# Kernel tuning notes

Measured on AMD Instinct MI355X. Metric: run time of the kernel, lower is better.

The kernel has to match this reference:

```python
import jax, jax.numpy as jnp
import numpy as np

# PyTorch LSTM cell with zero initial (h, c): W_hh @ h0 == 0, and c = sigmoid(i)*tanh(g)
# since the forget-gate term f*c0 vanishes. Gate order in torch: i, f, g, o.
# b here is the combined b_ih + b_hh (identical math).

def lstm_step0(x, Wih, b):
    pre = x @ Wih.T + b                      # (N, 4H)
    i, f, g, o = jnp.split(pre, 4, axis=-1)
    c = jax.nn.sigmoid(i) * jnp.tanh(g)
    return jax.nn.sigmoid(o) * jnp.tanh(c)   # (N, H)


def setup_inputs() -> dict:
    key = jax.random.key(0)
    ks = jax.random.split(key, 13)
    num_ts, num_periods, F = 128, 256, 128
    GH, NH, NF = 512, 256, 10
    s = lambda k, shape, fan: (jax.random.normal(k, shape, jnp.float32) / np.sqrt(fan))
    return {
        "X": jax.random.normal(ks[0], (num_ts, num_periods, F), jnp.float32),
        "g_Wih0": s(ks[1], (4 * GH, F), F),
        "g_b0": s(ks[2], (4 * GH,), GH),
        "g_Wih1": s(ks[3], (4 * GH, GH), GH),
        "g_b1": s(ks[4], (4 * GH,), GH),
        "aff_W": s(ks[5], (NF, GH), GH),
        "aff_b": s(ks[6], (NF,), GH),
        "n_Wih0": s(ks[7], (4 * NH, F), F),
        "n_b0": s(ks[8], (4 * NH,), NH),
        "n_Wih1": s(ks[9], (4 * NH, NH), NH),
        "n_b1": s(ks[10], (4 * NH,), NH),
        "noise_W": s(ks[11], (1, NH), NH),
        "noise_b": s(ks[12], (1,), NH),
    }


def reference(X, g_Wih0, g_b0, g_Wih1, g_b1, aff_W, aff_b,
              n_Wih0, n_b0, n_Wih1, n_b1, noise_W, noise_b):
    num_ts, num_periods, num_feats = X.shape
    x = X.reshape(-1, num_feats)             # (num_ts*num_periods, F)

    # Global factor branch: 2-layer LSTM single step from zero state
    hg = lstm_step0(lstm_step0(x, g_Wih0, g_b0), g_Wih1, g_b1)
    hg = jax.nn.relu(hg)
    mus = (hg @ aff_W.T + aff_b).sum(axis=-1).reshape(num_ts, num_periods)

    # Noise branch: 2-layer LSTM single step from zero state
    hn = lstm_step0(lstm_step0(x, n_Wih0, n_b0), n_Wih1, n_b1)
    hn = jax.nn.relu(hn)
    sigmas = jax.nn.softplus(hn @ noise_W.T + noise_b)  # log(1+exp(.)), stable
    sigmas = sigmas.reshape(num_ts, num_periods) + 1e-6
    return mus, sigmas
```

## Files before the change

### kernel.cpp

```cpp
#include <hip/hip_runtime.h>
#include <hip/hip_bf16.h>
#include <hip/hip_fp16.h>

typedef _Float16 h8_t __attribute__((ext_vector_type(8)));
typedef _Float16 h4_t __attribute__((ext_vector_type(4)));
typedef float f4_t __attribute__((ext_vector_type(4)));

#define M_ROWS 32768

__device__ __forceinline__ void gload_lds16(const void* g, void* l) {
  __builtin_amdgcn_global_load_lds((const __attribute__((address_space(1))) void*)g,
                                   (__attribute__((address_space(3))) void*)l, 16, 0, 0);
}

__device__ __forceinline__ float sigmoid_f(float x) { return 1.f / (1.f + __expf(-x)); }
__device__ __forceinline__ float tanh_f(float x) { return 1.f - 2.f / (__expf(2.f * x) + 1.f); }

struct GArgs {
  const _Float16* A;
  const _Float16* W;
  const float* bias;
  _Float16* Hout;
  const float* rvec;
  float* partial;
};

__global__ void prep_all(const float* __restrict__ X, const float* __restrict__ gW0,
                         const float* __restrict__ gW1, const float* __restrict__ nW0,
                         const float* __restrict__ nW1, const float* __restrict__ aff_W,
                         const float* __restrict__ aff_b,
                         _Float16* __restrict__ Xh, _Float16* __restrict__ Wg0,
                         _Float16* __restrict__ Wg1, _Float16* __restrict__ Wn0,
                         _Float16* __restrict__ Wn1,
                         float* __restrict__ pg, float* __restrict__ pn,
                         float* __restrict__ wsum) {
  int b = blockIdx.x;
  const float* s; _Float16* d; int base;
  if (b < 4096)      { s = X;   d = Xh;  base = b; }
  else if (b < 4352) { s = gW0; d = Wg0; base = b - 4096; }
  else if (b < 5376) { s = gW1; d = Wg1; base = b - 4352; }
  else if (b < 5504) { s = nW0; d = Wn0; base = b - 5376; }
  else if (b < 5760) { s = nW1; d = Wn1; base = b - 5504; }
  else if (b < 5888) {
    int i = (b - 5760) * 256 + threadIdx.x;
    pg[i] = 0.f; pn[i] = 0.f;
    return;
  } else {
    int j = (b - 5888) * 256 + threadIdx.x;
    float sum = 0.f;
#pragma unroll
    for (int r = 0; r < 10; ++r) sum += aff_W[r * 512 + j];
    wsum[j] = sum;
    if (j == 0) {
      float bs = 0.f;
#pragma unroll
      for (int r = 0; r < 10; ++r) bs += aff_b[r];
      wsum[512] = bs;
    }
    return;
  }
  int i4 = (base * 256 + threadIdx.x) * 4;
  float4 v = *(const float4*)(s + i4);
  h4_t o;
  o[0] = (_Float16)v.x; o[1] = (_Float16)v.y; o[2] = (_Float16)v.z; o[3] = (_Float16)v.w;
  *(h4_t*)(d + i4) = o;
}

template <int K_DIM, int H_DIM, bool FUSE>
__device__ __forceinline__ void gemm_body(const GArgs& ga, int h0, int m0,
                                          _Float16* As, _Float16* Bs) {
  const int tid = threadIdx.x;
  const int wid = tid >> 6;
  const int lane = tid & 63;
  const int wave_m = wid >> 1;
  const int wave_h = wid & 1;
  const int q = lane >> 4;
  const int tcol = lane & 15;

  constexpr int NT = K_DIM / 64;
  constexpr int A_BYTES = 128 * 64 * 2;
  constexpr int B_BYTES = 3 * 64 * 64 * 2;
  constexpr int A_ELEMS = 128 * 64;
  constexpr int B_ELEMS = 3 * 64 * 64;

  const _Float16* aptr[4]; int aoff[4];
#pragma unroll
  for (int c = 0; c < 4; ++c) {
    int o = ((wid * 4 + c) << 10) + (lane << 4);
    int row = o >> 7, pch = (o >> 4) & 7;
    int lch = pch ^ (row & 7);
    aptr[c] = ga.A + (size_t)(m0 + row) * K_DIM + lch * 8;
    aoff[c] = o;
  }
  const _Float16* bptr[6]; int boff[6];
#pragma unroll
  for (int c = 0; c < 6; ++c) {
    int o = ((wid * 6 + c) << 10) + (lane << 4);
    int pan = o >> 13;
    int row = (o >> 7) & 63, pch = (o >> 4) & 7;
    int lch = pch ^ (row & 7);
    int gbase = (pan == 0 ? 0 : (pan == 1 ? 2 * H_DIM : 3 * H_DIM)) + h0 + row;
    bptr[c] = ga.W + (size_t)gbase * K_DIM + lch * 8;
    boff[c] = o;
  }
  int a_rd[2][4];
#pragma unroll
  for (int ks = 0; ks < 2; ++ks)
#pragma unroll
    for (int mi = 0; mi < 4; ++mi) {
      int r = wave_m * 64 + mi * 16 + tcol;
      int c = ks * 4 + q;
      a_rd[ks][mi] = r * 64 + (c ^ (r & 7)) * 8;
    }
  int b_rd[2][2];
#pragma unroll
  for (int ks = 0; ks < 2; ++ks)
#pragma unroll
    for (int ni = 0; ni < 2; ++ni) {
      int j = wave_h * 32 + ni * 16 + tcol;
      int c = ks * 4 + q;
      b_rd[ks][ni] = j * 64 + (c ^ (j & 7)) * 8;
    }

  f4_t acc[3][4][2];
#pragma unroll
  for (int p = 0; p < 3; ++p)
#pragma unroll
    for (int mi = 0; mi < 4; ++mi)
#pragma unroll
      for (int ni = 0; ni < 2; ++ni) acc[p][mi][ni] = (f4_t){0.f, 0.f, 0.f, 0.f};

#pragma unroll
  for (int c = 0; c < 4; ++c) gload_lds16(aptr[c], (char*)As + aoff[c]);
#pragma unroll
  for (int c = 0; c < 6; ++c) gload_lds16(bptr[c], (char*)Bs + boff[c]);
#pragma unroll
  for (int c = 0; c < 4; ++c) aptr[c] += 64;
#pragma unroll
  for (int c = 0; c < 6; ++c) bptr[c] += 64;

#pragma unroll
  for (int kk = 0; kk < NT; ++kk) {
    const int cur = kk & 1;
    const int nxt = cur ^ 1;
    if (kk < NT - 1) {
#pragma unroll
      for (int c = 0; c < 4; ++c) gload_lds16(aptr[c], (char*)As + nxt * A_BYTES + aoff[c]);
#pragma unroll
      for (int c = 0; c < 6; ++c) gload_lds16(bptr[c], (char*)Bs + nxt * B_BYTES + boff[c]);
#pragma unroll
      for (int c = 0; c < 4; ++c) aptr[c] += 64;
#pragma unroll
      for (int c = 0; c < 6; ++c) bptr[c] += 64;
      asm volatile("s_waitcnt vmcnt(10)" ::: "memory");
    } else {
      asm volatile("s_waitcnt vmcnt(0)" ::: "memory");
    }
    __builtin_amdgcn_s_barrier();
    asm volatile("" ::: "memory");

#pragma unroll
    for (int ks = 0; ks < 2; ++ks) {
      h8_t af[4];
#pragma unroll
      for (int mi = 0; mi < 4; ++mi) af[mi] = *(const h8_t*)&As[cur * A_ELEMS + a_rd[ks][mi]];
#pragma unroll
      for (int p = 0; p < 3; ++p) {
#pragma unroll
        for (int ni = 0; ni < 2; ++ni) {
          h8_t bf = *(const h8_t*)&Bs[cur * B_ELEMS + p * 4096 + b_rd[ks][ni]];
#pragma unroll
          for (int mi = 0; mi < 4; ++mi)
            acc[p][mi][ni] = __builtin_amdgcn_mfma_f32_16x16x32_f16(af[mi], bf, acc[p][mi][ni], 0, 0, 0);
        }
      }
    }
    asm volatile("" ::: "memory");
    if (kk < NT - 1) __builtin_amdgcn_s_barrier();
  }

  const int mrow0 = m0 + wave_m * 64;
  const int jcol0 = h0 + wave_h * 32;

  if constexpr (!FUSE) {
#pragma unroll
    for (int ni = 0; ni < 2; ++ni) {
      int j = jcol0 + ni * 16 + tcol;
      float bi = ga.bias[j];
      float bg = ga.bias[2 * H_DIM + j];
      float bo = ga.bias[3 * H_DIM + j];
#pragma unroll
      for (int mi = 0; mi < 4; ++mi)
#pragma unroll
        for (int r = 0; r < 4; ++r) {
          float pi = acc[0][mi][ni][r] + bi;
          float pgt = acc[1][mi][ni][r] + bg;
          float po = acc[2][mi][ni][r] + bo;
          float cc = sigmoid_f(pi) * tanh_f(pgt);
          float hh = sigmoid_f(po) * tanh_f(cc);
          int m = mrow0 + mi * 16 + q * 4 + r;
          ga.Hout[(size_t)m * H_DIM + j] = (_Float16)hh;
        }
    }
  } else {
    float rsum[4][4];
#pragma unroll
    for (int mi = 0; mi < 4; ++mi)
#pragma unroll
      for (int r = 0; r < 4; ++r) rsum[mi][r] = 0.f;
#pragma unroll
    for (int ni = 0; ni < 2; ++ni) {
      int j = jcol0 + ni * 16 + tcol;
      float bi = ga.bias[j];
      float bg = ga.bias[2 * H_DIM + j];
      float bo = ga.bias[3 * H_DIM + j];
      float rv = ga.rvec[j];
#pragma unroll
      for (int mi = 0; mi < 4; ++mi)
#pragma unroll
        for (int r = 0; r < 4; ++r) {
          float pi = acc[0][mi][ni][r] + bi;
          float pgt = acc[1][mi][ni][r] + bg;
          float po = acc[2][mi][ni][r] + bo;
          float cc = sigmoid_f(pi) * tanh_f(pgt);
          float hh = sigmoid_f(po) * tanh_f(cc);
          hh = fmaxf(hh, 0.f);
          rsum[mi][r] += hh * rv;
        }
    }
#pragma unroll
    for (int mi = 0; mi < 4; ++mi)
#pragma unroll
      for (int r = 0; r < 4; ++r) {
        float v = rsum[mi][r];
        v += __shfl_xor(v, 1);
        v += __shfl_xor(v, 2);
        v += __shfl_xor(v, 4);
        v += __shfl_xor(v, 8);
        if (tcol == 0) atomicAdd(&ga.partial[mrow0 + mi * 16 + q * 4 + r], v);
      }
  }
}

__device__ __forceinline__ void swizzle_xy(int& x, int& y) {
  int lin = blockIdx.y * gridDim.x + blockIdx.x;
  int c = lin & 7;
  int r = lin >> 3;
  y = r % 12;
  x = c * 32 + r / 12;
}

__global__ __launch_bounds__(256, 2) void layer1_fused(GArgs g, GArgs n) {
  __shared__ __align__(16) _Float16 As[2 * 128 * 64];
  __shared__ __align__(16) _Float16 Bs[2 * 3 * 64 * 64];
  int x, y; swizzle_xy(x, y);
  if (y < 8) gemm_body<128, 512, false>(g, y * 64, x * 128, As, Bs);
  else       gemm_body<128, 256, false>(n, (y - 8) * 64, x * 128, As, Bs);
}

__global__ __launch_bounds__(256, 2) void layer2_fused(GArgs g, GArgs n) {
  __shared__ __align__(16) _Float16 As[2 * 128 * 64];
  __shared__ __align__(16) _Float16 Bs[2 * 3 * 64 * 64];
  int x, y; swizzle_xy(x, y);
  if (y < 8) gemm_body<512, 512, true>(g, y * 64, x * 128, As, Bs);
  else       gemm_body<256, 256, true>(n, (y - 8) * 64, x * 128, As, Bs);
}

__global__ void finalize(const float* __restrict__ pg, const float* __restrict__ pn,
                         const float* __restrict__ wsum, const float* __restrict__ noise_b,
                         float* __restrict__ out) {
  int i = blockIdx.x * blockDim.x + threadIdx.x;
  out[i] = pg[i] + wsum[512];
  float x = pn[i] + noise_b[0];
  float sp = fmaxf(x, 0.f) + log1pf(expf(-fabsf(x)));
  out[M_ROWS + i] = sp + 1e-6f;
}

extern "C" void kernel_launch(void* const* d_in, const int* in_sizes, int n_in,
                              void* d_out, int out_size, void* d_ws, size_t ws_size,
                              hipStream_t stream) {
  const float* X       = (const float*)d_in[0];
  const float* g_Wih0  = (const float*)d_in[1];
  const float* g_b0    = (const float*)d_in[2];
  const float* g_Wih1  = (const float*)d_in[3];
  const float* g_b1    = (const float*)d_in[4];
  const float* aff_W   = (const float*)d_in[5];
  const float* aff_b   = (const float*)d_in[6];
  const float* n_Wih0  = (const float*)d_in[7];
  const float* n_b0    = (const float*)d_in[8];
  const float* n_Wih1  = (const float*)d_in[9];
  const float* n_b1    = (const float*)d_in[10];
  const float* noise_W = (const float*)d_in[11];
  const float* noise_b = (const float*)d_in[12];
  float* out = (float*)d_out;

  char* w = (char*)d_ws;
  _Float16* Xh  = (_Float16*)w; w += (size_t)M_ROWS * 128 * 2;
  _Float16* Wg0 = (_Float16*)w; w += 2048 * 128 * 2;
  _Float16* Wg1 = (_Float16*)w; w += 2048 * 512 * 2;
  _Float16* Wn0 = (_Float16*)w; w += 1024 * 128 * 2;
  _Float16* Wn1 = (_Float16*)w; w += 1024 * 256 * 2;
  _Float16* h1g = (_Float16*)w; w += (size_t)M_ROWS * 512 * 2;
  _Float16* h1n = (_Float16*)w; w += (size_t)M_ROWS * 256 * 2;
  float* pg   = (float*)w; w += (size_t)M_ROWS * 4;
  float* pn   = (float*)w; w += (size_t)M_ROWS * 4;
  float* wsum = (float*)w; w += 4096;

  prep_all<<<5890, 256, 0, stream>>>(X, g_Wih0, g_Wih1, n_Wih0, n_Wih1, aff_W, aff_b,
                                     Xh, Wg0, Wg1, Wn0, Wn1, pg, pn, wsum);

  GArgs l1g = {Xh, Wg0, g_b0, h1g, nullptr, nullptr};
  GArgs l1n = {Xh, Wn0, n_b0, h1n, nullptr, nullptr};
  layer1_fused<<<dim3(M_ROWS / 128, 12), 256, 0, stream>>>(l1g, l1n);

  GArgs l2g = {h1g, Wg1, g_b1, nullptr, wsum, pg};
  GArgs l2n = {h1n, Wn1, n_b1, nullptr, noise_W, pn};
  layer2_fused<<<dim3(M_ROWS / 128, 12), 256, 0, stream>>>(l2g, l2n);

  finalize<<<M_ROWS / 256, 256, 0, stream>>>(pg, pn, wsum, noise_b, out);
}
```

Baseline: 274.3 us.

## Process two M-tiles per block with B-tile reuse and continuous prefetch pipeline

Each workgroup now walks two consecutive 128-row M tiles in one software-pipelined loop, so prefetching of the next tile's A overlaps the previous tile's epilogue. For layer 1 (K=128, NT=2), the B weight tiles stay resident in LDS and are not reloaded for the second M tile. Bias and rvec loads are hoisted out of the epilogue. The grid is halved to 128x12 blocks, which lowers per-block launch overhead but also reduces parallelism and adds epilogue work inside the main loop.

```diff
diff --git a/kernel.cpp b/kernel.cpp
--- a/kernel.cpp
+++ b/kernel.cpp
@@ -66,8 +66,8 @@
   *(h4_t*)(d + i4) = o;
 }
 
-template <int K_DIM, int H_DIM, bool FUSE>
-__device__ __forceinline__ void gemm_body(const GArgs& ga, int h0, int m0,
+template <int K_DIM, int H_DIM, bool FUSE, int NMT>
+__device__ __forceinline__ void gemm_body(const GArgs& ga, int h0, int m_base,
                                           _Float16* As, _Float16* Bs) {
   const int tid = threadIdx.x;
   const int wid = tid >> 6;
@@ -78,6 +78,8 @@
   const int tcol = lane & 15;
 
   constexpr int NT = K_DIM / 64;
+  constexpr int TOT = NMT * NT;
+  constexpr bool BREUSE = (NT == 2);
   constexpr int A_BYTES = 128 * 64 * 2;
   constexpr int B_BYTES = 3 * 64 * 64 * 2;
   constexpr int A_ELEMS = 128 * 64;
@@ -89,7 +91,7 @@
     int o = ((wid * 4 + c) << 10) + (lane << 4);
     int row = o >> 7, pch = (o >> 4) & 7;
     int lch = pch ^ (row & 7);
-    aptr[c] = ga.A + (size_t)(m0 + row) * K_DIM + lch * 8;
+    aptr[c] = ga.A + (size_t)(m_base + row) * K_DIM + lch * 8;
     aoff[c] = o;
   }
   const _Float16* bptr[6]; int boff[6];
@@ -122,6 +124,17 @@
       b_rd[ks][ni] = j * 64 + (c ^ (j & 7)) * 8;
     }
 
+  const int jcol0 = h0 + wave_h * 32;
+  float ebi[2], ebg[2], ebo[2], erv[2];
+#pragma unroll
+  for (int ni = 0; ni < 2; ++ni) {
+    int j = jcol0 + ni * 16 + tcol;
+    ebi[ni] = ga.bias[j];
+    ebg[ni] = ga.bias[2 * H_DIM + j];
+    ebo[ni] = ga.bias[3 * H_DIM + j];
+    erv[ni] = FUSE ? ga.rvec[j] : 0.f;
+  }
+
   f4_t acc[3][4][2];
 #pragma unroll
   for (int p = 0; p < 3; ++p)
@@ -140,19 +153,35 @@
   for (int c = 0; c < 6; ++c) bptr[c] += 64;
 
 #pragma unroll
-  for (int kk = 0; kk < NT; ++kk) {
-    const int cur = kk & 1;
+  for (int s = 0; s < TOT; ++s) {
+    const int cur = s & 1;
     const int nxt = cur ^ 1;
-    if (kk < NT - 1) {
+    if (s < TOT - 1) {
+      const bool stB = (!BREUSE) || (s + 1 < NT);
 #pragma unroll
       for (int c = 0; c < 4; ++c) gload_lds16(aptr[c], (char*)As + nxt * A_BYTES + aoff[c]);
-#pragma unroll
-      for (int c = 0; c < 6; ++c) gload_lds16(bptr[c], (char*)Bs + nxt * B_BYTES + boff[c]);
-#pragma unroll
-      for (int c = 0; c < 4; ++c) aptr[c] += 64;
-#pragma unroll
-      for (int c = 0; c < 6; ++c) bptr[c] += 64;
-      asm volatile("s_waitcnt vmcnt(10)" ::: "memory");
+      if (stB) {
+#pragma unroll
+        for (int c = 0; c < 6; ++c) gload_lds16(bptr[c], (char*)Bs + nxt * B_BYTES + boff[c]);
+      }
+      if (((s + 2) % NT) == 0) {
+#pragma unroll
+        for (int c = 0; c < 4; ++c) aptr[c] += 128 * K_DIM - (NT - 1) * 64;
+      } else {
+#pragma unroll
+        for (int c = 0; c < 4; ++c) aptr[c] += 64;
+      }
+      if (stB) {
+        if (((s + 2) % NT) == 0) {
+#pragma unroll
+          for (int c = 0; c < 6; ++c) bptr[c] -= (NT - 1) * 64;
+        } else {
+#pragma unroll
+          for (int c = 0; c < 6; ++c) bptr[c] += 64;
+        }
+      }
+      if (stB) asm volatile("s_waitcnt vmcnt(10)" ::: "memory");
+      else     asm volatile("s_waitcnt vmcnt(4)" ::: "memory");
     } else {
       asm volatile("s_waitcnt vmcnt(0)" ::: "memory");
     }
@@ -176,69 +205,69 @@
       }
     }
     asm volatile("" ::: "memory");
-    if (kk < NT - 1) __builtin_amdgcn_s_barrier();
-  }
-
-  const int mrow0 = m0 + wave_m * 64;
-  const int jcol0 = h0 + wave_h * 32;
-
-  if constexpr (!FUSE) {
-#pragma unroll
-    for (int ni = 0; ni < 2; ++ni) {
-      int j = jcol0 + ni * 16 + tcol;
-      float bi = ga.bias[j];
-      float bg = ga.bias[2 * H_DIM + j];
-      float bo = ga.bias[3 * H_DIM + j];
-#pragma unroll
-      for (int mi = 0; mi < 4; ++mi)
-#pragma unroll
-        for (int r = 0; r < 4; ++r) {
-          float pi = acc[0][mi][ni][r] + bi;
-          float pgt = acc[1][mi][ni][r] + bg;
-          float po = acc[2][mi][ni][r] + bo;
-          float cc = sigmoid_f(pi) * tanh_f(pgt);
-          float hh = sigmoid_f(po) * tanh_f(cc);
-          int m = mrow0 + mi * 16 + q * 4 + r;
-          ga.Hout[(size_t)m * H_DIM + j] = (_Float16)hh;
+
+    if ((s % NT) == NT - 1) {
+      const int mm = s / NT;
+      const int mrow0 = m_base + mm * 128 + wave_m * 64;
+      if constexpr (!FUSE) {
+#pragma unroll
+        for (int ni = 0; ni < 2; ++ni) {
+          int j = jcol0 + ni * 16 + tcol;
+#pragma unroll
+          for (int mi = 0; mi < 4; ++mi)
+#pragma unroll
+            for (int r = 0; r < 4; ++r) {
+              float pi = acc[0][mi][ni][r] + ebi[ni];
+              float pgt = acc[1][mi][ni][r] + ebg[ni];
+              float po = acc[2][mi][ni][r] + ebo[ni];
+              float cc = sigmoid_f(pi) * tanh_f(pgt);
+              float hh = sigmoid_f(po) * tanh_f(cc);
+              int m = mrow0 + mi * 16 + q * 4 + r;
+              ga.Hout[(size_t)m * H_DIM + j] = (_Float16)hh;
+            }
         }
-    }
-  } else {
-    float rsum[4][4];
-#pragma unroll
-    for (int mi = 0; mi < 4; ++mi)
-#pragma unroll
-      for (int r = 0; r < 4; ++r) rsum[mi][r] = 0.f;
-#pragma unroll
-    for (int ni = 0; ni < 2; ++ni) {
-      int j = jcol0 + ni * 16 + tcol;
-      float bi = ga.bias[j];
-      float bg = ga.bias[2 * H_DIM + j];
-      float bo = ga.bias[3 * H_DIM + j];
-      float rv = ga.rvec[j];
-#pragma unroll
-      for (int mi = 0; mi < 4; ++mi)
-#pragma unroll
-        for (int r = 0; r < 4; ++r) {
-          float pi = acc[0][mi][ni][r] + bi;
-          float pgt = acc[1][mi][ni][r] + bg;
-          float po = acc[2][mi][ni][r] + bo;
-          float cc = sigmoid_f(pi) * tanh_f(pgt);
-          float hh = sigmoid_f(po) * tanh_f(cc);
-          hh = fmaxf(hh, 0.f);
-          rsum[mi][r] += hh * rv;
+      } else {
+        float rsum[4][4];
+#pragma unroll
+        for (int mi = 0; mi < 4; ++mi)
+#pragma unroll
+          for (int r = 0; r < 4; ++r) rsum[mi][r] = 0.f;
+#pragma unroll
+        for (int ni = 0; ni < 2; ++ni) {
+#pragma unroll
+          for (int mi = 0; mi < 4; ++mi)
+#pragma unroll
+            for (int r = 0; r < 4; ++r) {
+              float pi = acc[0][mi][ni][r] + ebi[ni];
+              float pgt = acc[1][mi][ni][r] + ebg[ni];
+              float po = acc[2][mi][ni][r] + ebo[ni];
+              float cc = sigmoid_f(pi) * tanh_f(pgt);
+              float hh = sigmoid_f(po) * tanh_f(cc);
+              hh = fmaxf(hh, 0.f);
+              rsum[mi][r] += hh * erv[ni];
+            }
         }
-    }
-#pragma unroll
-    for (int mi = 0; mi < 4; ++mi)
-#pragma unroll
-      for (int r = 0; r < 4; ++r) {
-        float v = rsum[mi][r];
-        v += __shfl_xor(v, 1);
-        v += __shfl_xor(v, 2);
-        v += __shfl_xor(v, 4);
-        v += __shfl_xor(v, 8);
-        if (tcol == 0) atomicAdd(&ga.partial[mrow0 + mi * 16 + q * 4 + r], v);
-      }
+#pragma unroll
+        for (int mi = 0; mi < 4; ++mi)
+#pragma unroll
+          for (int r = 0; r < 4; ++r) {
+            float v = rsum[mi][r];
+            v += __shfl_xor(v, 1);
+            v += __shfl_xor(v, 2);
+            v += __shfl_xor(v, 4);
+            v += __shfl_xor(v, 8);
+            if (tcol == 0) atomicAdd(&ga.partial[mrow0 + mi * 16 + q * 4 + r], v);
+          }
+      }
+#pragma unroll
+      for (int p = 0; p < 3; ++p)
+#pragma unroll
+        for (int mi = 0; mi < 4; ++mi)
+#pragma unroll
+          for (int ni = 0; ni < 2; ++ni) acc[p][mi][ni] = (f4_t){0.f, 0.f, 0.f, 0.f};
+    }
+
+    if (s < TOT - 1) __builtin_amdgcn_s_barrier();
   }
 }
 
@@ -247,23 +276,23 @@
   int c = lin & 7;
   int r = lin >> 3;
   y = r % 12;
-  x = c * 32 + r / 12;
+  x = c * 16 + r / 12;
 }
 
 __global__ __launch_bounds__(256, 2) void layer1_fused(GArgs g, GArgs n) {
   __shared__ __align__(16) _Float16 As[2 * 128 * 64];
   __shared__ __align__(16) _Float16 Bs[2 * 3 * 64 * 64];
   int x, y; swizzle_xy(x, y);
-  if (y < 8) gemm_body<128, 512, false>(g, y * 64, x * 128, As, Bs);
-  else       gemm_body<128, 256, false>(n, (y - 8) * 64, x * 128, As, Bs);
+  if (y < 8) gemm_body<128, 512, false, 2>(g, y * 64, x * 256, As, Bs);
+  else       gemm_body<128, 256, false, 2>(n, (y - 8) * 64, x * 256, As, Bs);
 }
 
 __global__ __launch_bounds__(256, 2) void layer2_fused(GArgs g, GArgs n) {
   __shared__ __align__(16) _Float16 As[2 * 128 * 64];
   __shared__ __align__(16) _Float16 Bs[2 * 3 * 64 * 64];
   int x, y; swizzle_xy(x, y);
-  if (y < 8) gemm_body<512, 512, true>(g, y * 64, x * 128, As, Bs);
-  else       gemm_body<256, 256, true>(n, (y - 8) * 64, x * 128, As, Bs);
+  if (y < 8) gemm_body<512, 512, true, 2>(g, y * 64, x * 256, As, Bs);
+  else       gemm_body<256, 256, true, 2>(n, (y - 8) * 64, x * 256, As, Bs);
 }
 
 __global__ void finalize(const float* __restrict__ pg, const float* __restrict__ pn,
@@ -311,11 +340,11 @@
 
   GArgs l1g = {Xh, Wg0, g_b0, h1g, nullptr, nullptr};
   GArgs l1n = {Xh, Wn0, n_b0, h1n, nullptr, nullptr};
-  layer1_fused<<<dim3(M_ROWS / 128, 12), 256, 0, stream>>>(l1g, l1n);
+  layer1_fused<<<dim3(128, 12), 256, 0, stream>>>(l1g, l1n);
 
   GArgs l2g = {h1g, Wg1, g_b1, nullptr, wsum, pg};
   GArgs l2n = {h1n, Wn1, n_b1, nullptr, noise_W, pn};
-  layer2_fused<<<dim3(M_ROWS / 128, 12), 256, 0, stream>>>(l2g, l2n);
+  layer2_fused<<<dim3(128, 12), 256, 0, stream>>>(l2g, l2n);
 
   finalize<<<M_ROWS / 256, 256, 0, stream>>>(pg, pn, wsum, noise_b, out);
 }
```

Result: no change. 273.6 us (-0.2%).
